# Kernel optimization log

Measured on AMD Instinct MI355X. Metric: run time of the kernel, lower is better.

The kernel has to match this reference:

```python
import jax, jax.numpy as jnp
import numpy as np

B, S, D = 8, 1024, 768
H, HD = 12, 64  # heads, head dim (H*HD == D)
EPS = 1e-12


def setup_inputs() -> dict:
    key = jax.random.key(0)
    ks = jax.random.split(key, 8)
    s = 0.02
    return {
        "hidden_states": jax.random.normal(ks[0], (B, S, D), jnp.float32),
        "attention_mask": jnp.zeros((B, 1, 1, S), jnp.float32),
        "head_mask": jnp.ones((H,), jnp.float32),
        "Wq": jax.random.normal(ks[1], (D, H * HD), jnp.float32) * s,
        "bq": jnp.zeros((H * HD,), jnp.float32),
        "Wk": jax.random.normal(ks[2], (D, H * HD), jnp.float32) * s,
        "bk": jnp.zeros((H * HD,), jnp.float32),
        "Wv": jax.random.normal(ks[3], (D, H * HD), jnp.float32) * s,
        "bv": jnp.zeros((H * HD,), jnp.float32),
        "Wo": jax.random.normal(ks[4], (D, H * HD), jnp.float32) * s,  # torch Linear weight [out=D, in=H*HD]
        "bo": jnp.zeros((D,), jnp.float32),
        "gamma": jnp.ones((D,), jnp.float32),
        "beta": jnp.zeros((D,), jnp.float32),
    }


def reference(hidden_states, attention_mask, head_mask, Wq, bq, Wk, bk, Wv, bv, Wo, bo, gamma, beta):
    def heads(x):  # [B,S,H*HD] -> [B,H,S,HD]
        return x.reshape(B, S, H, HD).transpose(0, 2, 1, 3)

    q = heads(hidden_states @ Wq.T + bq)
    k = heads(hidden_states @ Wk.T + bk)
    v = heads(hidden_states @ Wv.T + bv)

    scores = jnp.einsum("bhqd,bhkd->bhqk", q, k) / np.sqrt(HD).astype(np.float32)
    scores = scores + attention_mask
    probs = jax.nn.softmax(scores, axis=-1)  # dropout p=0 (eval)
    ctx = jnp.einsum("bhqk,bhkd->bhqd", probs, v)  # [B,H,S,HD]

    # masked per-head output projection: Wo.T.view(H, HD, D)
    Wph = Wo.T.reshape(H, HD, D)
    proj = jnp.einsum("bhsd,hde,h->bse", ctx, Wph, head_mask) + bo

    # residual + LayerNorm
    x = proj + hidden_states
    mu = jnp.mean(x, axis=-1, keepdims=True)
    var = jnp.mean(jnp.square(x - mu), axis=-1, keepdims=True)
    out = (x - mu) * jax.lax.rsqrt(var + EPS) * gamma + beta
    return out
```

## Files before the change

### kernel.cpp

```cpp
#include <hip/hip_runtime.h>
#include <math.h>

#define Bn 8
#define Sn 1024
#define Dn 768
#define Hn 12
#define MROWS (Bn * Sn)

typedef __attribute__((ext_vector_type(8))) short short8;
typedef __attribute__((ext_vector_type(4))) float floatx4;

__device__ __forceinline__ unsigned short f2b(float x) {
    union { float f; unsigned u; } v; v.f = x;
    unsigned r = v.u + 0x7fffu + ((v.u >> 16) & 1u);
    return (unsigned short)(r >> 16);
}

__device__ __forceinline__ void gload16(const void* g, void* l) {
    __builtin_amdgcn_global_load_lds(
        (const __attribute__((address_space(1))) void*)g,
        (__attribute__((address_space(3))) void*)l, 16, 0, 0);
}

__global__ __launch_bounds__(256) void convert_bf16(const float* __restrict__ in,
                                                    unsigned short* __restrict__ out, int n4) {
    int i = blockIdx.x * 256 + threadIdx.x;
    if (i >= n4) return;
    float4 v = reinterpret_cast<const float4*>(in)[i];
    ushort4 o;
    o.x = f2b(v.x); o.y = f2b(v.y); o.z = f2b(v.z); o.w = f2b(v.w);
    reinterpret_cast<ushort4*>(out)[i] = o;
}

__global__ __launch_bounds__(256) void convert_w4(const float* __restrict__ a, const float* __restrict__ b,
                                                  const float* __restrict__ c, const float* __restrict__ d,
                                                  unsigned short* __restrict__ oa, unsigned short* __restrict__ ob,
                                                  unsigned short* __restrict__ oc, unsigned short* __restrict__ od,
                                                  int n4) {
    int i = blockIdx.x * 256 + threadIdx.x;
    if (i >= n4) return;
    const int y = blockIdx.y;
    const float* src = (y == 0) ? a : (y == 1) ? b : (y == 2) ? c : d;
    unsigned short* dst = (y == 0) ? oa : (y == 1) ? ob : (y == 2) ? oc : od;
    float4 v = reinterpret_cast<const float4*>(src)[i];
    ushort4 o;
    o.x = f2b(v.x); o.y = f2b(v.y); o.z = f2b(v.z); o.w = f2b(v.w);
    reinterpret_cast<ushort4*>(dst)[i] = o;
}

__global__ __launch_bounds__(256) void gemm_qkv(const unsigned short* __restrict__ A,
                                                const unsigned short* __restrict__ Wq,
                                                const unsigned short* __restrict__ Wk,
                                                const unsigned short* __restrict__ Wv,
                                                const float* __restrict__ bq,
                                                const float* __restrict__ bk,
                                                const float* __restrict__ bv,
                                                unsigned short* __restrict__ Qh,
                                                unsigned short* __restrict__ Kh,
                                                unsigned short* __restrict__ Vt) {
    __shared__ __align__(16) unsigned short As[128 * 32];
    __shared__ __align__(16) unsigned short Ws[128 * 32];
    const int id = blockIdx.x;
    const int by = id & 63;
    const int bx = id >> 6;
    const int mat = bx / 6;
    const int m0 = by * 128;
    const int n0 = (bx % 6) * 128;
    const unsigned short* W = (mat == 0) ? Wq : (mat == 1) ? Wk : Wv;
    const float* bias = (mat == 0) ? bq : (mat == 1) ? bk : bv;
    unsigned short* Cout = (mat == 0) ? Qh : (mat == 1) ? Kh : Vt;

    const int tid = threadIdx.x;
    const int w = tid >> 6, l = tid & 63, quad = l >> 4, mr = l & 15;
    const int wm = (w >> 1) * 64, wn = (w & 1) * 64;

    const unsigned short* gA0 = &A[(size_t)(m0 + w * 32 + (l >> 2)) * Dn + (l & 3) * 8];
    const unsigned short* gA1 = gA0 + 16 * Dn;
    const unsigned short* gW0 = &W[(size_t)(n0 + w * 32 + (l >> 2)) * Dn + (l & 3) * 8];
    const unsigned short* gW1 = gW0 + 16 * Dn;
    unsigned short* lA0 = &As[w * 1024];
    unsigned short* lA1 = &As[w * 1024 + 512];
    unsigned short* lW0 = &Ws[w * 1024];
    unsigned short* lW1 = &Ws[w * 1024 + 512];

    floatx4 acc[4][4];
#pragma unroll
    for (int i = 0; i < 4; i++)
#pragma unroll
        for (int j = 0; j < 4; j++) {
            floatx4 z = {0.f, 0.f, 0.f, 0.f};
            acc[i][j] = z;
        }

    for (int k0 = 0; k0 < Dn; k0 += 32) {
        __syncthreads();
        gload16(gA0 + k0, lA0);
        gload16(gA1 + k0, lA1);
        gload16(gW0 + k0, lW0);
        gload16(gW1 + k0, lW1);
        __syncthreads();
        short8 af[4], bfr[4];
#pragma unroll
        for (int i = 0; i < 4; i++)
            af[i] = *(const short8*)&As[(wm + i * 16 + mr) * 32 + quad * 8];
#pragma unroll
        for (int j = 0; j < 4; j++)
            bfr[j] = *(const short8*)&Ws[(wn + j * 16 + mr) * 32 + quad * 8];
#pragma unroll
        for (int i = 0; i < 4; i++)
#pragma unroll
            for (int j = 0; j < 4; j++)
                acc[i][j] = __builtin_amdgcn_mfma_f32_16x16x32_bf16(af[i], bfr[j], acc[i][j], 0, 0, 0);
    }

#pragma unroll
    for (int j = 0; j < 4; j++) {
        const int col = n0 + wn + j * 16 + mr;
        const float bval = bias[col];
        const int h = col >> 6, d = col & 63;
#pragma unroll
        for (int i = 0; i < 4; i++) {
#pragma unroll
            for (int r = 0; r < 4; r++) {
                const int m = m0 + wm + i * 16 + quad * 4 + r;
                const float val = acc[i][j][r] + bval;
                const int b = m >> 10, s = m & 1023;
                const size_t base = (size_t)(b * Hn + h) << 16;
                if (mat == 2)
                    Cout[base + (size_t)d * 1024 + s] = f2b(val);
                else
                    Cout[base + (size_t)s * 64 + d] = f2b(val);
            }
        }
    }
}

__global__ __launch_bounds__(256) void gemm_out(const unsigned short* __restrict__ A,
                                                const unsigned short* __restrict__ W,
                                                const float* __restrict__ bias,
                                                const float* __restrict__ X,
                                                float* __restrict__ xres) {
    __shared__ __align__(16) unsigned short As[128 * 32];
    __shared__ __align__(16) unsigned short Ws[128 * 32];
    const int id = blockIdx.x;
    const int by = id & 63;
    const int bx = id >> 6;
    const int m0 = by * 128;
    const int n0 = bx * 128;

    const int tid = threadIdx.x;
    const int w = tid >> 6, l = tid & 63, quad = l >> 4, mr = l & 15;
    const int wm = (w >> 1) * 64, wn = (w & 1) * 64;

    const unsigned short* gA0 = &A[(size_t)(m0 + w * 32 + (l >> 2)) * Dn + (l & 3) * 8];
    const unsigned short* gA1 = gA0 + 16 * Dn;
    const unsigned short* gW0 = &W[(size_t)(n0 + w * 32 + (l >> 2)) * Dn + (l & 3) * 8];
    const unsigned short* gW1 = gW0 + 16 * Dn;
    unsigned short* lA0 = &As[w * 1024];
    unsigned short* lA1 = &As[w * 1024 + 512];
    unsigned short* lW0 = &Ws[w * 1024];
    unsigned short* lW1 = &Ws[w * 1024 + 512];

    floatx4 acc[4][4];
#pragma unroll
    for (int i = 0; i < 4; i++)
#pragma unroll
        for (int j = 0; j < 4; j++) {
            floatx4 z = {0.f, 0.f, 0.f, 0.f};
            acc[i][j] = z;
        }

    for (int k0 = 0; k0 < Dn; k0 += 32) {
        __syncthreads();
        gload16(gA0 + k0, lA0);
        gload16(gA1 + k0, lA1);
        gload16(gW0 + k0, lW0);
        gload16(gW1 + k0, lW1);
        __syncthreads();
        short8 af[4], bfr[4];
#pragma unroll
        for (int i = 0; i < 4; i++)
            af[i] = *(const short8*)&As[(wm + i * 16 + mr) * 32 + quad * 8];
#pragma unroll
        for (int j = 0; j < 4; j++)
            bfr[j] = *(const short8*)&Ws[(wn + j * 16 + mr) * 32 + quad * 8];
#pragma unroll
        for (int i = 0; i < 4; i++)
#pragma unroll
            for (int j = 0; j < 4; j++)
                acc[i][j] = __builtin_amdgcn_mfma_f32_16x16x32_bf16(af[i], bfr[j], acc[i][j], 0, 0, 0);
    }

#pragma unroll
    for (int j = 0; j < 4; j++) {
        const int col = n0 + wn + j * 16 + mr;
        const float bval = bias[col];
#pragma unroll
        for (int i = 0; i < 4; i++) {
#pragma unroll
            for (int r = 0; r < 4; r++) {
                const int m = m0 + wm + i * 16 + quad * 4 + r;
                xres[(size_t)m * Dn + col] = acc[i][j][r] + bval + X[(size_t)m * Dn + col];
            }
        }
    }
}

__global__ __launch_bounds__(256) void flash_attn_mfma(const unsigned short* __restrict__ Qh,
                                                       const unsigned short* __restrict__ Kh,
                                                       const unsigned short* __restrict__ Vt,
                                                       const float* __restrict__ mask,
                                                       const float* __restrict__ head_mask,
                                                       unsigned short* __restrict__ ctx) {
    __shared__ __align__(16) unsigned short Ks[64 * 72];
    __shared__ __align__(16) unsigned short Vs[64 * 72];
    __shared__ __align__(16) unsigned short Ps[128 * 72];
    __shared__ float msk[64];

    const int id = blockIdx.x;
    const int bh = id % 96;
    const int qt = id / 96;
    const int b = bh / Hn, h = bh % Hn;
    const int q0 = qt * 128;
    const int tid = threadIdx.x;
    const int w = tid >> 6, l = tid & 63, quad = l >> 4, mr = l & 15;
    const size_t hb = (size_t)(b * Hn + h) << 16;

    short8 aq[2][2];
#pragma unroll
    for (int i = 0; i < 2; i++)
#pragma unroll
        for (int ks = 0; ks < 2; ks++)
            aq[i][ks] = *(const short8*)&Qh[hb + (size_t)(q0 + w * 32 + i * 16 + mr) * 64 + ks * 32 + quad * 8];

    float l_s[2][4];
    floatx4 oacc[2][4];
#pragma unroll
    for (int i = 0; i < 2; i++) {
#pragma unroll
        for (int r = 0; r < 4; r++) l_s[i][r] = 0.f;
#pragma unroll
        for (int jj = 0; jj < 4; jj++) {
            floatx4 z = {0.f, 0.f, 0.f, 0.f};
            oacc[i][jj] = z;
        }
    }

    const int srow = tid >> 2;
    const int scol = (tid & 3) * 16;

    for (int kt = 0; kt < Sn / 64; kt++) {
        const int k0 = kt * 64;
        __syncthreads();
        *(short8*)&Ks[srow * 72 + scol] = *(const short8*)&Kh[hb + (size_t)(k0 + srow) * 64 + scol];
        *(short8*)&Ks[srow * 72 + scol + 8] = *(const short8*)&Kh[hb + (size_t)(k0 + srow) * 64 + scol + 8];
        *(short8*)&Vs[srow * 72 + scol] = *(const short8*)&Vt[hb + (size_t)srow * 1024 + k0 + scol];
        *(short8*)&Vs[srow * 72 + scol + 8] = *(const short8*)&Vt[hb + (size_t)srow * 1024 + k0 + scol + 8];
        if (tid < 64) msk[tid] = mask[b * Sn + k0 + tid];
        __syncthreads();

        floatx4 sacc[2][4];
#pragma unroll
        for (int i = 0; i < 2; i++)
#pragma unroll
            for (int j = 0; j < 4; j++) {
                floatx4 z = {0.f, 0.f, 0.f, 0.f};
                sacc[i][j] = z;
            }
#pragma unroll
        for (int ks = 0; ks < 2; ks++) {
#pragma unroll
            for (int j = 0; j < 4; j++) {
                short8 bk = *(const short8*)&Ks[(j * 16 + mr) * 72 + ks * 32 + quad * 8];
                sacc[0][j] = __builtin_amdgcn_mfma_f32_16x16x32_bf16(aq[0][ks], bk, sacc[0][j], 0, 0, 0);
                sacc[1][j] = __builtin_amdgcn_mfma_f32_16x16x32_bf16(aq[1][ks], bk, sacc[1][j], 0, 0, 0);
            }
        }

#pragma unroll
        for (int i = 0; i < 2; i++) {
#pragma unroll
            for (int j = 0; j < 4; j++) {
                const float mk = msk[j * 16 + mr];
#pragma unroll
                for (int r = 0; r < 4; r++) {
                    const float p = __expf(sacc[i][j][r] * 0.125f + mk);
                    l_s[i][r] += p;
                    Ps[(w * 32 + i * 16 + quad * 4 + r) * 72 + j * 16 + mr] = f2b(p);
                }
            }
        }

#pragma unroll
        for (int ks = 0; ks < 2; ks++) {
            short8 ap0 = *(const short8*)&Ps[(w * 32 + mr) * 72 + ks * 32 + quad * 8];
            short8 ap1 = *(const short8*)&Ps[(w * 32 + 16 + mr) * 72 + ks * 32 + quad * 8];
#pragma unroll
            for (int jj = 0; jj < 4; jj++) {
                short8 bv = *(const short8*)&Vs[(jj * 16 + mr) * 72 + ks * 32 + quad * 8];
                oacc[0][jj] = __builtin_amdgcn_mfma_f32_16x16x32_bf16(ap0, bv, oacc[0][jj], 0, 0, 0);
                oacc[1][jj] = __builtin_amdgcn_mfma_f32_16x16x32_bf16(ap1, bv, oacc[1][jj], 0, 0, 0);
            }
        }
    }

    const float hm = head_mask[h];
    float inv[2][4];
#pragma unroll
    for (int i = 0; i < 2; i++)
#pragma unroll
        for (int r = 0; r < 4; r++) {
            float t = l_s[i][r];
            t += __shfl_xor(t, 1);
            t += __shfl_xor(t, 2);
            t += __shfl_xor(t, 4);
            t += __shfl_xor(t, 8);
            inv[i][r] = hm / t;
        }
#pragma unroll
    for (int i = 0; i < 2; i++)
#pragma unroll
        for (int jj = 0; jj < 4; jj++)
#pragma unroll
            for (int r = 0; r < 4; r++) {
                const int qrow = q0 + w * 32 + i * 16 + quad * 4 + r;
                ctx[(size_t)(b * Sn + qrow) * Dn + h * 64 + jj * 16 + mr] = f2b(oacc[i][jj][r] * inv[i][r]);
            }
}

__global__ __launch_bounds__(256) void ln_kernel(const float* __restrict__ x,
                                                 const float* __restrict__ gamma,
                                                 const float* __restrict__ beta,
                                                 float* __restrict__ out) {
    __shared__ float r1[256];
    __shared__ float r2[256];
    const int m = blockIdx.x;
    const int tid = threadIdx.x;

    float xv[3];
    float s = 0.f, ss = 0.f;
#pragma unroll
    for (int i = 0; i < 3; i++) {
        int j = tid + i * 256;
        float t = x[(size_t)m * Dn + j];
        xv[i] = t;
        s += t;
        ss += t * t;
    }
    r1[tid] = s;
    r2[tid] = ss;
    __syncthreads();
    for (int off = 128; off > 0; off >>= 1) {
        if (tid < off) {
            r1[tid] += r1[tid + off];
            r2[tid] += r2[tid + off];
        }
        __syncthreads();
    }
    const float mu = r1[0] * (1.0f / Dn);
    const float var = r2[0] * (1.0f / Dn) - mu * mu;
    const float rstd = rsqrtf(var + 1e-12f);
#pragma unroll
    for (int i = 0; i < 3; i++) {
        int j = tid + i * 256;
        out[(size_t)m * Dn + j] = (xv[i] - mu) * rstd * gamma[j] + beta[j];
    }
}

extern "C" void kernel_launch(void* const* d_in, const int* in_sizes, int n_in,
                              void* d_out, int out_size, void* d_ws, size_t ws_size,
                              hipStream_t stream) {
    const float* X         = (const float*)d_in[0];
    const float* mask      = (const float*)d_in[1];
    const float* head_mask = (const float*)d_in[2];
    const float* Wq        = (const float*)d_in[3];
    const float* bq        = (const float*)d_in[4];
    const float* Wk        = (const float*)d_in[5];
    const float* bk        = (const float*)d_in[6];
    const float* Wv        = (const float*)d_in[7];
    const float* bv        = (const float*)d_in[8];
    const float* Wo        = (const float*)d_in[9];
    const float* bo        = (const float*)d_in[10];
    const float* gamma     = (const float*)d_in[11];
    const float* beta      = (const float*)d_in[12];
    float* out = (float*)d_out;

    const size_t NE = (size_t)Bn * Sn * Dn;
    const size_t NW = (size_t)Dn * Dn;

    char* p = (char*)d_ws;
    unsigned short* Xb  = (unsigned short*)p;  p += NE * 2;
    unsigned short* Wqb = (unsigned short*)p;  p += NW * 2;
    unsigned short* Wkb = (unsigned short*)p;  p += NW * 2;
    unsigned short* Wvb = (unsigned short*)p;  p += NW * 2;
    unsigned short* Wob = (unsigned short*)p;  p += NW * 2;
    unsigned short* Qh  = (unsigned short*)p;  p += NE * 2;
    unsigned short* Kh  = (unsigned short*)p;  p += NE * 2;
    unsigned short* Vtb = (unsigned short*)p;  p += NE * 2;
    unsigned short* ctx = (unsigned short*)p;  p += NE * 2;
    float* xres = (float*)p;

    convert_bf16<<<(int)(NE / 4 + 255) / 256, 256, 0, stream>>>(X, Xb, (int)(NE / 4));
    dim3 cw((unsigned)((NW / 4 + 255) / 256), 4);
    convert_w4<<<cw, 256, 0, stream>>>(Wq, Wk, Wv, Wo, Wqb, Wkb, Wvb, Wob, (int)(NW / 4));

    gemm_qkv<<<1152, 256, 0, stream>>>(Xb, Wqb, Wkb, Wvb, bq, bk, bv, Qh, Kh, Vtb);

    flash_attn_mfma<<<768, 256, 0, stream>>>(Qh, Kh, Vtb, mask, head_mask, ctx);

    gemm_out<<<384, 256, 0, stream>>>(ctx, Wob, bo, X, xres);

    ln_kernel<<<MROWS, 256, 0, stream>>>(xres, gamma, beta, out);
}
```

Before: 237.7 us.

## Double-buffer GEMM tiles, prefetch attention K/V, merge convert kernels, shrink out-proj tile

Merges the two fp32-to-bf16 conversion kernels into one launch. Both GEMMs now double-buffer their LDS tiles so the next k-slice's global-to-LDS load is issued before the current slice's MFMAs, which removes one barrier per iteration. The output projection drops to 64-row tiles, doubling the grid to 768 blocks for better CU occupancy. The attention kernel prefetches the next K/V/mask tile into registers while computing on the current one. The cost is more LDS and register pressure. The double-buffer path depends on the async LDS load having landed by the next barrier, with no explicit vmcnt wait.

```diff
diff --git a/kernel.cpp b/kernel.cpp
--- a/kernel.cpp
+++ b/kernel.cpp
@@ -22,26 +22,25 @@
         (__attribute__((address_space(3))) void*)l, 16, 0, 0);
 }
 
-__global__ __launch_bounds__(256) void convert_bf16(const float* __restrict__ in,
-                                                    unsigned short* __restrict__ out, int n4) {
-    int i = blockIdx.x * 256 + threadIdx.x;
-    if (i >= n4) return;
-    float4 v = reinterpret_cast<const float4*>(in)[i];
-    ushort4 o;
-    o.x = f2b(v.x); o.y = f2b(v.y); o.z = f2b(v.z); o.w = f2b(v.w);
-    reinterpret_cast<ushort4*>(out)[i] = o;
-}
-
-__global__ __launch_bounds__(256) void convert_w4(const float* __restrict__ a, const float* __restrict__ b,
-                                                  const float* __restrict__ c, const float* __restrict__ d,
-                                                  unsigned short* __restrict__ oa, unsigned short* __restrict__ ob,
-                                                  unsigned short* __restrict__ oc, unsigned short* __restrict__ od,
-                                                  int n4) {
-    int i = blockIdx.x * 256 + threadIdx.x;
-    if (i >= n4) return;
-    const int y = blockIdx.y;
-    const float* src = (y == 0) ? a : (y == 1) ? b : (y == 2) ? c : d;
-    unsigned short* dst = (y == 0) ? oa : (y == 1) ? ob : (y == 2) ? oc : od;
+__global__ __launch_bounds__(256) void convert_all(const float* __restrict__ X,
+                                                   const float* __restrict__ Wq, const float* __restrict__ Wk,
+                                                   const float* __restrict__ Wv, const float* __restrict__ Wo,
+                                                   unsigned short* __restrict__ Xb,
+                                                   unsigned short* __restrict__ Wqb, unsigned short* __restrict__ Wkb,
+                                                   unsigned short* __restrict__ Wvb, unsigned short* __restrict__ Wob) {
+    const int id = blockIdx.x;
+    const float* src;
+    unsigned short* dst;
+    int i;
+    if (id < 6144) {
+        src = X; dst = Xb;
+        i = id * 256 + threadIdx.x;
+    } else {
+        const int y = (id - 6144) / 576;
+        src = (y == 0) ? Wq : (y == 1) ? Wk : (y == 2) ? Wv : Wo;
+        dst = (y == 0) ? Wqb : (y == 1) ? Wkb : (y == 2) ? Wvb : Wob;
+        i = ((id - 6144) % 576) * 256 + threadIdx.x;
+    }
     float4 v = reinterpret_cast<const float4*>(src)[i];
     ushort4 o;
     o.x = f2b(v.x); o.y = f2b(v.y); o.z = f2b(v.z); o.w = f2b(v.w);
@@ -58,8 +57,8 @@
                                                 unsigned short* __restrict__ Qh,
                                                 unsigned short* __restrict__ Kh,
                                                 unsigned short* __restrict__ Vt) {
-    __shared__ __align__(16) unsigned short As[128 * 32];
-    __shared__ __align__(16) unsigned short Ws[128 * 32];
+    __shared__ __align__(16) unsigned short As[2][128 * 32];
+    __shared__ __align__(16) unsigned short Ws[2][128 * 32];
     const int id = blockIdx.x;
     const int by = id & 63;
     const int bx = id >> 6;
@@ -78,10 +77,7 @@
     const unsigned short* gA1 = gA0 + 16 * Dn;
     const unsigned short* gW0 = &W[(size_t)(n0 + w * 32 + (l >> 2)) * Dn + (l & 3) * 8];
     const unsigned short* gW1 = gW0 + 16 * Dn;
-    unsigned short* lA0 = &As[w * 1024];
-    unsigned short* lA1 = &As[w * 1024 + 512];
-    unsigned short* lW0 = &Ws[w * 1024];
-    unsigned short* lW1 = &Ws[w * 1024 + 512];
+    const int lo = w * 1024;
 
     floatx4 acc[4][4];
 #pragma unroll
@@ -92,20 +88,29 @@
             acc[i][j] = z;
         }
 
-    for (int k0 = 0; k0 < Dn; k0 += 32) {
+    gload16(gA0, &As[0][lo]);
+    gload16(gA1, &As[0][lo + 512]);
+    gload16(gW0, &Ws[0][lo]);
+    gload16(gW1, &Ws[0][lo + 512]);
+
+    for (int kt = 0; kt < 24; kt++) {
+        const int cur = kt & 1;
         __syncthreads();
-        gload16(gA0 + k0, lA0);
-        gload16(gA1 + k0, lA1);
-        gload16(gW0 + k0, lW0);
-        gload16(gW1 + k0, lW1);
-        __syncthreads();
+        if (kt < 23) {
+            const int k0 = (kt + 1) * 32;
+            const int nxt = cur ^ 1;
+            gload16(gA0 + k0, &As[nxt][lo]);
+            gload16(gA1 + k0, &As[nxt][lo + 512]);
+            gload16(gW0 + k0, &Ws[nxt][lo]);
+            gload16(gW1 + k0, &Ws[nxt][lo + 512]);
+        }
         short8 af[4], bfr[4];
 #pragma unroll
         for (int i = 0; i < 4; i++)
-            af[i] = *(const short8*)&As[(wm + i * 16 + mr) * 32 + quad * 8];
+            af[i] = *(const short8*)&As[cur][(wm + i * 16 + mr) * 32 + quad * 8];
 #pragma unroll
         for (int j = 0; j < 4; j++)
-            bfr[j] = *(const short8*)&Ws[(wn + j * 16 + mr) * 32 + quad * 8];
+            bfr[j] = *(const short8*)&Ws[cur][(wn + j * 16 + mr) * 32 + quad * 8];
 #pragma unroll
         for (int i = 0; i < 4; i++)
 #pragma unroll
@@ -140,66 +145,69 @@
                                                 const float* __restrict__ bias,
                                                 const float* __restrict__ X,
                                                 float* __restrict__ xres) {
-    __shared__ __align__(16) unsigned short As[128 * 32];
-    __shared__ __align__(16) unsigned short Ws[128 * 32];
+    __shared__ __align__(16) unsigned short As[2][64 * 32];
+    __shared__ __align__(16) unsigned short Ws[2][128 * 32];
     const int id = blockIdx.x;
-    const int by = id & 63;
-    const int bx = id >> 6;
-    const int m0 = by * 128;
+    const int by = id & 127;
+    const int bx = id >> 7;
+    const int m0 = by * 64;
     const int n0 = bx * 128;
 
     const int tid = threadIdx.x;
     const int w = tid >> 6, l = tid & 63, quad = l >> 4, mr = l & 15;
-    const int wm = (w >> 1) * 64, wn = (w & 1) * 64;
-
-    const unsigned short* gA0 = &A[(size_t)(m0 + w * 32 + (l >> 2)) * Dn + (l & 3) * 8];
-    const unsigned short* gA1 = gA0 + 16 * Dn;
+
+    const unsigned short* gA0 = &A[(size_t)(m0 + w * 16 + (l >> 2)) * Dn + (l & 3) * 8];
     const unsigned short* gW0 = &W[(size_t)(n0 + w * 32 + (l >> 2)) * Dn + (l & 3) * 8];
     const unsigned short* gW1 = gW0 + 16 * Dn;
-    unsigned short* lA0 = &As[w * 1024];
-    unsigned short* lA1 = &As[w * 1024 + 512];
-    unsigned short* lW0 = &Ws[w * 1024];
-    unsigned short* lW1 = &Ws[w * 1024 + 512];
-
-    floatx4 acc[4][4];
+    const int loA = w * 512;
+    const int loW = w * 1024;
+
+    floatx4 acc[4][2];
 #pragma unroll
     for (int i = 0; i < 4; i++)
 #pragma unroll
-        for (int j = 0; j < 4; j++) {
+        for (int j = 0; j < 2; j++) {
             floatx4 z = {0.f, 0.f, 0.f, 0.f};
             acc[i][j] = z;
         }
 
-    for (int k0 = 0; k0 < Dn; k0 += 32) {
+    gload16(gA0, &As[0][loA]);
+    gload16(gW0, &Ws[0][loW]);
+    gload16(gW1, &Ws[0][loW + 512]);
+
+    for (int kt = 0; kt < 24; kt++) {
+        const int cur = kt & 1;
         __syncthreads();
-        gload16(gA0 + k0, lA0);
-        gload16(gA1 + k0, lA1);
-        gload16(gW0 + k0, lW0);
-        gload16(gW1 + k0, lW1);
-        __syncthreads();
-        short8 af[4], bfr[4];
+        if (kt < 23) {
+            const int k0 = (kt + 1) * 32;
+            const int nxt = cur ^ 1;
+            gload16(gA0 + k0, &As[nxt][loA]);
+            gload16(gW0 + k0, &Ws[nxt][loW]);
+            gload16(gW1 + k0, &Ws[nxt][loW + 512]);
+        }
+        short8 af[4], bfr[2];
 #pragma unroll
         for (int i = 0; i < 4; i++)
-            af[i] = *(const short8*)&As[(wm + i * 16 + mr) * 32 + quad * 8];
-#pragma unroll
-        for (int j = 0; j < 4; j++)
-            bfr[j] = *(const short8*)&Ws[(wn + j * 16 + mr) * 32 + quad * 8];
+            af[i] = *(const short8*)&As[cur][(i * 16 + mr) * 32 + quad * 8];
+#pragma unroll
+        for (int j = 0; j < 2; j++)
+            bfr[j] = *(const short8*)&Ws[cur][(w * 32 + j * 16 + mr) * 32 + quad * 8];
 #pragma unroll
         for (int i = 0; i < 4; i++)
 #pragma unroll
-            for (int j = 0; j < 4; j++)
+            for (int j = 0; j < 2; j++)
                 acc[i][j] = __builtin_amdgcn_mfma_f32_16x16x32_bf16(af[i], bfr[j], acc[i][j], 0, 0, 0);
     }
 
 #pragma unroll
-    for (int j = 0; j < 4; j++) {
-        const int col = n0 + wn + j * 16 + mr;
+    for (int j = 0; j < 2; j++) {
+        const int col = n0 + w * 32 + j * 16 + mr;
         const float bval = bias[col];
 #pragma unroll
         for (int i = 0; i < 4; i++) {
 #pragma unroll
             for (int r = 0; r < 4; r++) {
-                const int m = m0 + wm + i * 16 + quad * 4 + r;
+                const int m = m0 + i * 16 + quad * 4 + r;
                 xres[(size_t)m * Dn + col] = acc[i][j][r] + bval + X[(size_t)m * Dn + col];
             }
         }
@@ -249,14 +257,27 @@
     const int srow = tid >> 2;
     const int scol = (tid & 3) * 16;
 
+    short8 pk0 = *(const short8*)&Kh[hb + (size_t)srow * 64 + scol];
+    short8 pk1 = *(const short8*)&Kh[hb + (size_t)srow * 64 + scol + 8];
+    short8 pv0 = *(const short8*)&Vt[hb + (size_t)srow * 1024 + scol];
+    short8 pv1 = *(const short8*)&Vt[hb + (size_t)srow * 1024 + scol + 8];
+    float pm = mask[b * Sn + (tid & 63)];
+
     for (int kt = 0; kt < Sn / 64; kt++) {
-        const int k0 = kt * 64;
         __syncthreads();
-        *(short8*)&Ks[srow * 72 + scol] = *(const short8*)&Kh[hb + (size_t)(k0 + srow) * 64 + scol];
-        *(short8*)&Ks[srow * 72 + scol + 8] = *(const short8*)&Kh[hb + (size_t)(k0 + srow) * 64 + scol + 8];
-        *(short8*)&Vs[srow * 72 + scol] = *(const short8*)&Vt[hb + (size_t)srow * 1024 + k0 + scol];
-        *(short8*)&Vs[srow * 72 + scol + 8] = *(const short8*)&Vt[hb + (size_t)srow * 1024 + k0 + scol + 8];
-        if (tid < 64) msk[tid] = mask[b * Sn + k0 + tid];
+        *(short8*)&Ks[srow * 72 + scol] = pk0;
+        *(short8*)&Ks[srow * 72 + scol + 8] = pk1;
+        *(short8*)&Vs[srow * 72 + scol] = pv0;
+        *(short8*)&Vs[srow * 72 + scol + 8] = pv1;
+        if (tid < 64) msk[tid] = pm;
+        if (kt < Sn / 64 - 1) {
+            const int k0 = (kt + 1) * 64;
+            pk0 = *(const short8*)&Kh[hb + (size_t)(k0 + srow) * 64 + scol];
+            pk1 = *(const short8*)&Kh[hb + (size_t)(k0 + srow) * 64 + scol + 8];
+            pv0 = *(const short8*)&Vt[hb + (size_t)srow * 1024 + k0 + scol];
+            pv1 = *(const short8*)&Vt[hb + (size_t)srow * 1024 + k0 + scol + 8];
+            pm = mask[b * Sn + k0 + (tid & 63)];
+        }
         __syncthreads();
 
         floatx4 sacc[2][4];
@@ -400,15 +421,13 @@
     unsigned short* ctx = (unsigned short*)p;  p += NE * 2;
     float* xres = (float*)p;
 
-    convert_bf16<<<(int)(NE / 4 + 255) / 256, 256, 0, stream>>>(X, Xb, (int)(NE / 4));
-    dim3 cw((unsigned)((NW / 4 + 255) / 256), 4);
-    convert_w4<<<cw, 256, 0, stream>>>(Wq, Wk, Wv, Wo, Wqb, Wkb, Wvb, Wob, (int)(NW / 4));
+    convert_all<<<8448, 256, 0, stream>>>(X, Wq, Wk, Wv, Wo, Xb, Wqb, Wkb, Wvb, Wob);
 
     gemm_qkv<<<1152, 256, 0, stream>>>(Xb, Wqb, Wkb, Wvb, bq, bk, bv, Qh, Kh, Vtb);
 
     flash_attn_mfma<<<768, 256, 0, stream>>>(Qh, Kh, Vtb, mask, head_mask, ctx);
 
-    gemm_out<<<384, 256, 0, stream>>>(ctx, Wob, bo, X, xres);
+    gemm_out<<<768, 256, 0, stream>>>(ctx, Wob, bo, X, xres);
 
     ln_kernel<<<MROWS, 256, 0, stream>>>(xres, gamma, beta, out);
 }
```

New measurement: 244.4 us. 2.8% more time.
